# Optimization experiments

Hardware: AMD Instinct MI355X
Metric: run time of the kernel (lower is better)

## Reference

```python
import jax, jax.numpy as jnp
import numpy as np
import math

IMG = 224
PATCH = 14
E = 1024          # transformer width (ViT-L/14)
H = 16            # num heads
DH = E // H       # head dim
LAYERS = 24
FF = 4 * E        # CLIP MLP hidden
NROI = 32         # number of ROI bboxes
NSIDE = IMG // PATCH
NPATCH = NSIDE * NSIDE  # 256
T = 1 + NPATCH    # sequence length incl. CLS
INIT = 0.02
EPS_LN = 1e-5


def setup_inputs() -> dict:
    key = jax.random.key(0)
    ks = jax.random.split(key, 16)
    frame = jax.random.uniform(ks[0], (3, IMG, IMG), dtype=jnp.float32)
    # valid bboxes in pixel coords: x1<x2, y1<y2
    c = jax.random.uniform(ks[1], (NROI, 2), dtype=jnp.float32) * (IMG - 40.0) + 20.0
    s = jax.random.uniform(ks[2], (NROI, 2), dtype=jnp.float32) * 60.0 + 20.0
    bboxes = jnp.stack([c[:, 0] - s[:, 0] / 2, c[:, 1] - s[:, 1] / 2,
                        c[:, 0] + s[:, 0] / 2, c[:, 1] + s[:, 1] / 2], axis=-1)
    bboxes = jnp.clip(bboxes, 0.0, float(IMG))
    f32 = jnp.float32
    conv_w = jax.random.normal(ks[3], (E, 3, PATCH, PATCH), f32) * INIT
    cls_emb = jax.random.normal(ks[4], (E,), f32) * INIT
    wq = jax.random.normal(ks[5], (LAYERS, E, E), f32) * INIT
    wk = jax.random.normal(ks[6], (LAYERS, E, E), f32) * INIT
    wv = jax.random.normal(ks[7], (LAYERS, E, E), f32) * INIT
    wo = jax.random.normal(ks[8], (LAYERS, E, E), f32) * INIT
    bq = jnp.zeros((LAYERS, E), f32); bk = jnp.zeros((LAYERS, E), f32)
    bv = jnp.zeros((LAYERS, E), f32); bo = jnp.zeros((LAYERS, E), f32)
    ln1_s = jnp.ones((LAYERS, E), f32); ln1_b = jnp.zeros((LAYERS, E), f32)
    ln2_s = jnp.ones((LAYERS, E), f32); ln2_b = jnp.zeros((LAYERS, E), f32)
    w1 = jax.random.normal(ks[9], (LAYERS, E, FF), f32) * INIT
    b1 = jnp.zeros((LAYERS, FF), f32)
    w2 = jax.random.normal(ks[10], (LAYERS, FF, E), f32) * INIT
    b2 = jnp.zeros((LAYERS, E), f32)
    return {"frame": frame, "bboxes": bboxes, "conv_w": conv_w, "cls_emb": cls_emb,
            "ln1_s": ln1_s, "ln1_b": ln1_b, "wq": wq, "bq": bq, "wk": wk, "bk": bk,
            "wv": wv, "bv": bv, "wo": wo, "bo": bo, "ln2_s": ln2_s, "ln2_b": ln2_b,
            "w1": w1, "b1": b1, "w2": w2, "b2": b2}


def _patch_coords():
    r = jnp.arange(NSIDE, dtype=jnp.float32)
    c = jnp.arange(NSIDE, dtype=jnp.float32)
    cc, rr = jnp.meshgrid(c, r)  # row-major like the python loop
    x1 = (cc * PATCH).reshape(-1); y1 = (rr * PATCH).reshape(-1)
    return jnp.stack([x1, y1, x1 + PATCH, y1 + PATCH], axis=-1)  # (NPATCH,4)


def _overlap_ratio(bboxes, patches):
    # intersection area / patch area -> Mi (N, NPATCH)
    bx1, by1, bx2, by2 = [bboxes[:, None, i] for i in range(4)]
    px1, py1, px2, py2 = [patches[None, :, i] for i in range(4)]
    iw = jnp.clip(jnp.minimum(bx2, px2) - jnp.maximum(bx1, px1), 0.0)
    ih = jnp.clip(jnp.minimum(by2, py2) - jnp.maximum(by1, py1), 0.0)
    parea = (px2 - px1) * (py2 - py1)
    return iw * ih / parea


def _ln(x, s, b):
    m = jnp.mean(x, axis=-1, keepdims=True)
    v = jnp.var(x, axis=-1, keepdims=True)
    return (x - m) * jax.lax.rsqrt(v + EPS_LN) * s + b


def _quick_gelu(x):
    return x * jax.nn.sigmoid(1.702 * x)


def _forward(frame, bboxes, conv_w, cls_emb, ln1_s, ln1_b, wq, bq, wk, bk,
             wv, bv, wo, bo, ln2_s, ln2_b, w1, b1, w2, b2):
    # patch embed: conv stride=PATCH, then relu (as in module forward)
    x = jax.lax.conv_general_dilated(frame[None], conv_w, (PATCH, PATCH), 'VALID',
                                     dimension_numbers=('NCHW', 'OIHW', 'NCHW'))
    x = jax.nn.relu(x)                      # (1, E, NSIDE, NSIDE)
    x = x.reshape(E, NPATCH).T              # (NPATCH, E)
    x = jnp.concatenate([cls_emb[None, :], x], axis=0)  # (T, E)

    Mi = _overlap_ratio(bboxes, _patch_coords())  # (NROI, NPATCH)
    pb = Mi.sum(axis=0)
    pb = pb / (pb.max() + 1e-6)
    attn_bias = jnp.zeros((T, T), jnp.float32).at[0, 1:].set(pb)

    scale = 1.0 / math.sqrt(DH)

    def blk(x, p):
        l1s, l1b, Wq, Bq, Wk, Bk, Wv, Bv, Wo, Bo, l2s, l2b, W1, B1, W2, B2 = p
        h = _ln(x, l1s, l1b)
        q = (h @ Wq + Bq).reshape(T, H, DH)
        k = (h @ Wk + Bk).reshape(T, H, DH)
        v = (h @ Wv + Bv).reshape(T, H, DH)
        scores = jnp.einsum('lhd,shd->hls', q, k) * scale + attn_bias[None]
        a = jax.nn.softmax(scores, axis=-1)
        o = jnp.einsum('hls,shd->lhd', a, v).reshape(T, E) @ Wo + Bo
        x = x + o
        h2 = _ln(x, l2s, l2b)
        m = _quick_gelu(h2 @ W1 + B1) @ W2 + B2
        return x + m, None

    x, _ = jax.lax.scan(blk, x, (ln1_s, ln1_b, wq, bq, wk, bk, wv, bv, wo, bo,
                                 ln2_s, ln2_b, w1, b1, w2, b2))

    cls_out = x[0:1]            # (1, E)
    patch_out = x[1:]           # (NPATCH, E)
    roi = Mi @ patch_out        # (NROI, E)
    return jnp.concatenate([cls_out, roi], axis=0)  # (1+NROI, E)


def reference(frame, bboxes, conv_w, cls_emb, ln1_s, ln1_b, wq, bq, wk, bk,
              wv, bv, wo, bo, ln2_s, ln2_b, w1, b1, w2, b2):
    return _forward(frame, bboxes, conv_w, cls_emb, ln1_s, ln1_b, wq, bq, wk, bk,
                    wv, bv, wo, bo, ln2_s, ln2_b, w1, b1, w2, b2)
```

## Files before the change

kernel.cpp:

```cpp
#include <hip/hip_runtime.h>
#include <hip/hip_bf16.h>
#include <math.h>

#define E_DIM 1024
#define FF_DIM 4096
#define LAYERS 24
#define MPAD 384
#define SPAD 288
#define KCP 608

typedef __attribute__((ext_vector_type(8))) short short8;
typedef __attribute__((ext_vector_type(8))) __bf16 bf16x8;
typedef __attribute__((ext_vector_type(4))) float float4_t;
typedef __attribute__((ext_vector_type(4))) unsigned short ushort4_t;

union ABu { short8 s; bf16x8 b; };
union BFU { __bf16 b; unsigned short u; };

__device__ __forceinline__ float4_t MFMAs(short8 a, short8 b, float4_t c) {
  ABu ua, ub; ua.s = a; ub.s = b;
  return __builtin_amdgcn_mfma_f32_16x16x32_bf16(ua.b, ub.b, c, 0, 0, 0);
}
__device__ __forceinline__ unsigned short f2bf(float f) {
  BFU x; x.b = (__bf16)f; return x.u;
}

__global__ void prep_kernel(const float* __restrict__ frame, const float* __restrict__ conv_w,
                            unsigned short* __restrict__ Pm, unsigned short* __restrict__ Wp,
                            unsigned short* __restrict__ h, unsigned short* __restrict__ ob,
                            unsigned short* __restrict__ vTb) {
  int b = blockIdx.x, tid = threadIdx.x;
  if (b < 256) {
    int pr = b >> 4, pc = b & 15;
    for (int kk = tid; kk < KCP; kk += 256) {
      unsigned short us = 0;
      if (kk < 588) {
        int c = kk / 196, rem = kk % 196;
        int i = rem / 14, j = rem % 14;
        us = f2bf(frame[c * 224 * 224 + (pr * 14 + i) * 224 + (pc * 14 + j)]);
      }
      Pm[b * KCP + kk] = us;
    }
  } else if (b < 1280) {
    int n = b - 256;
    for (int kk = tid; kk < KCP; kk += 256) {
      unsigned short us = (kk < 588) ? f2bf(conv_w[n * 588 + kk]) : (unsigned short)0;
      Wp[n * KCP + kk] = us;
    }
  } else {
    int idx = (b - 1280) * 256 + tid;
    const int NH = (MPAD - 257) * E_DIM;
    const int NO = (MPAD - 272) * E_DIM;
    const int NV = 16 * 64 * (SPAD - 272);
    if (idx < NH) {
      h[257 * E_DIM + idx] = 0;
    } else if (idx < NH + NO) {
      ob[272 * E_DIM + (idx - NH)] = 0;
    } else if (idx < NH + NO + NV) {
      int i = idx - NH - NO;
      vTb[(size_t)(i >> 4) * SPAD + 272 + (i & 15)] = 0;
    }
  }
}

__global__ void pb_cls_kernel(const float* __restrict__ bboxes, const float* __restrict__ cls_emb,
                              float* __restrict__ pb, float* __restrict__ Mi, float* __restrict__ x) {
  __shared__ float sb[128];
  __shared__ float red[256];
  int tid = threadIdx.x;
  if (tid < 128) sb[tid] = bboxes[tid];
  __syncthreads();
  int p = tid;
  float px1 = (float)((p & 15) * 14), py1 = (float)((p >> 4) * 14);
  float px2 = px1 + 14.f, py2 = py1 + 14.f;
  float s = 0.f;
  for (int r = 0; r < 32; ++r) {
    float bx1 = sb[r * 4 + 0], by1 = sb[r * 4 + 1], bx2 = sb[r * 4 + 2], by2 = sb[r * 4 + 3];
    float iw = fmaxf(fminf(bx2, px2) - fmaxf(bx1, px1), 0.f);
    float ih = fmaxf(fminf(by2, py2) - fmaxf(by1, py1), 0.f);
    float ov = iw * ih * (1.f / 196.f);
    Mi[r * 256 + p] = ov;
    s += ov;
  }
  red[tid] = s;
  __syncthreads();
  for (int off = 128; off > 0; off >>= 1) {
    if (tid < off) red[tid] = fmaxf(red[tid], red[tid + off]);
    __syncthreads();
  }
  pb[p] = s / (red[0] + 1e-6f);
  for (int j = 0; j < 4; ++j) x[tid * 4 + j] = cls_emb[tid * 4 + j];
}

__global__ __launch_bounds__(256) void conv_gemm(const unsigned short* __restrict__ Pm,
                                                 const unsigned short* __restrict__ Wp,
                                                 float* __restrict__ x) {
  int n0 = blockIdx.x * 16;
  int tid = threadIdx.x, wave = tid >> 6, lane = tid & 63;
  int lg = lane >> 4, lc = lane & 15;
  float4_t acc[4] = {{0,0,0,0},{0,0,0,0},{0,0,0,0},{0,0,0,0}};
  const unsigned short* bp = Wp + (size_t)(n0 + lc) * KCP + lg * 8;
  const unsigned short* apt[4];
#pragma unroll
  for (int t = 0; t < 4; ++t) apt[t] = Pm + (size_t)((wave + t * 4) * 16 + lc) * KCP + lg * 8;
  for (int s = 0; s < 19; ++s) {
    short8 bf = *(const short8*)bp; bp += 32;
#pragma unroll
    for (int t = 0; t < 4; ++t) {
      short8 af = *(const short8*)apt[t]; apt[t] += 32;
      acc[t] = MFMAs(af, bf, acc[t]);
    }
  }
#pragma unroll
  for (int t = 0; t < 4; ++t) {
    int mbase = (wave + t * 4) * 16 + lg * 4;
#pragma unroll
    for (int r = 0; r < 4; ++r)
      x[(size_t)(1 + mbase + r) * E_DIM + n0 + lc] = fmaxf(acc[t][r], 0.f);
  }
}

#define WAITB(n) asm volatile("s_waitcnt vmcnt(" #n ") lgkmcnt(0)\n\ts_barrier" ::: "memory")
#define WAITV(n) asm volatile("s_waitcnt vmcnt(" #n ")" ::: "memory")

template <int NTOT, int EPI, int NK>
__global__ __launch_bounds__(256, 1) void gemm_nk(
    const unsigned short* __restrict__ A, int lda,
    const float* __restrict__ Wa, const float* __restrict__ Wb2, const float* __restrict__ Wc,
    const float* __restrict__ ba, const float* __restrict__ bb, const float* __restrict__ bc,
    int NNT,
    unsigned short* __restrict__ oq, unsigned short* __restrict__ okk,
    unsigned short* __restrict__ ovT, unsigned short* __restrict__ om,
    float* __restrict__ opart) {
  static_assert(NK == 2 || NK >= 3, "NK>=2");
  __shared__ __align__(16) char WbT[3 * 8192];
  int b = blockIdx.x;
  int p = ((b >> 4) << 3) | (b & 7);
  int mh = (b >> 3) & 1;
  int nt = p % NNT, ks = p / NNT;

  int tid = threadIdx.x, wave = tid >> 6, lane = tid & 63;
  int lg = lane >> 4, lc = lane & 15;

  const float* W; const float* bias; int ncl;
  if (EPI == 0) {
    int sel = nt >> 5; ncl = (nt & 31) << 5;
    W = (sel == 0) ? Wa : ((sel == 1) ? Wb2 : Wc);
    bias = (sel == 0) ? ba : ((sel == 1) ? bb : bc);
  } else {
    ncl = nt << 5; W = Wa; bias = ba;
  }

  const int kb0 = ks * (NK * 128);

  const int scol = tid & 31, rg = tid >> 5;
  const int skey = (scol & 7) * 16;
  const float* gsrc = W + (size_t)(kb0 + rg * 16) * NTOT + ncl + scol;
  const int wo0 = scol * 256 + ((rg * 32) ^ skey);
  const int wo1 = scol * 256 + ((rg * 32 + 16) ^ skey);

  const unsigned short* ap[3];
#pragma unroll
  for (int j = 0; j < 3; ++j) {
    int t0 = mh * 12 + wave * 3 + j;
    ap[j] = A + (size_t)(t0 * 16 + lc) * lda + kb0 + lg * 8;
  }

  float4_t acc[6];
#pragma unroll
  for (int i = 0; i < 6; ++i) acc[i] = (float4_t){0, 0, 0, 0};

  float g[2][16];
  short8 av[2][12];
  const int keyr = (lc & 7) * 16;

#define ISSUE_G(slot, t) { _Pragma("unroll") for (int j = 0; j < 16; ++j) \
    g[slot][j] = gsrc[(size_t)(t) * 128 * NTOT + (size_t)j * NTOT]; }
#define ISSUE_A(slot, t) { _Pragma("unroll") for (int s = 0; s < 4; ++s) \
    _Pragma("unroll") for (int j = 0; j < 3; ++j) \
      av[slot][s * 3 + j] = *(const short8*)(ap[j] + (size_t)(t) * 128 + s * 32); }
#define WRITE_G(slot, t) { short8 wlo, whi; \
    _Pragma("unroll") for (int j = 0; j < 8; ++j) { \
      wlo[j] = (short)f2bf(g[slot][j]); whi[j] = (short)f2bf(g[slot][8 + j]); } \
    char* dstb = WbT + ((t) % 3) * 8192; \
    *(short8*)(dstb + wo0) = wlo; \
    *(short8*)(dstb + wo1) = whi; }
#define COMP(t) { const char* ldsb = WbT + ((t) % 3) * 8192; \
    _Pragma("unroll") for (int s = 0; s < 4; ++s) { \
      int o = (s * 64 + lg * 16) ^ keyr; \
      short8 wf0 = *(const short8*)(ldsb + lc * 256 + o); \
      short8 wf1 = *(const short8*)(ldsb + (lc + 16) * 256 + o); \
      _Pragma("unroll") for (int j = 0; j < 3; ++j) { \
        acc[j * 2 + 0] = MFMAs(wf0, av[(t) & 1][s * 3 + j], acc[j * 2 + 0]); \
        acc[j * 2 + 1] = MFMAs(wf1, av[(t) & 1][s * 3 + j], acc[j * 2 + 1]); } } }

  if constexpr (NK == 2) {
    ISSUE_G(0, 0) ISSUE_G(1, 1) ISSUE_A(0, 0) ISSUE_A(1, 1)
    WAITV(24);
    WRITE_G(0, 0) WRITE_G(1, 1)
    asm volatile("s_waitcnt lgkmcnt(0)\n\ts_barrier" ::: "memory");
    WAITV(12);
    COMP(0)
    WAITV(0);
    COMP(1)
  } else {
    ISSUE_G(0, 0) ISSUE_G(1, 1) ISSUE_A(0, 0)
    WAITV(28);
    WRITE_G(0, 0)
    ISSUE_G(0, 2) ISSUE_A(1, 1)
#pragma unroll
    for (int t = 0; t < NK; ++t) {
      if (t <= NK - 3)      { WAITB(28); }
      else if (t == NK - 2) { WAITB(12); }
      else                  { WAITB(0);  }
      if (t + 1 < NK) WRITE_G((t + 1) & 1, t + 1)
      COMP(t)
      if (t + 3 < NK) ISSUE_G((t + 3) & 1, t + 3)
      if (t + 2 < NK) ISSUE_A(t & 1, t + 2)
    }
  }
#undef ISSUE_G
#undef ISSUE_A
#undef WRITE_G
#undef COMP

  float4_t bv0 = {0,0,0,0}, bv1 = {0,0,0,0};
  if (bias) {
    bv0 = *(const float4_t*)(bias + ncl + lg * 4);
    bv1 = *(const float4_t*)(bias + ncl + 16 + lg * 4);
  }

  if (EPI == 0) {
    int sel = nt >> 5;
    int head = ncl >> 6;
    int db0 = (ncl & 63) + lg * 4;
    int db1 = (ncl & 63) + 16 + lg * 4;
#pragma unroll
    for (int j = 0; j < 3; ++j) {
      int tile = mh * 12 + wave * 3 + j;
      int m = tile * 16 + lc;
      if (sel < 2) {
        unsigned short* dst = (sel == 0 ? oq : okk) + ((size_t)(head * MPAD + m)) * 64;
        ushort4_t h0, h1;
#pragma unroll
        for (int r = 0; r < 4; ++r) {
          h0[r] = f2bf(acc[j * 2 + 0][r] + bv0[r]);
          h1[r] = f2bf(acc[j * 2 + 1][r] + bv1[r]);
        }
        *(ushort4_t*)(dst + db0) = h0;
        *(ushort4_t*)(dst + db1) = h1;
      } else if (tile < 17) {
#pragma unroll
        for (int r = 0; r < 4; ++r) {
          ovT[(size_t)(head * 64 + db0 + r) * SPAD + m] = f2bf(acc[j * 2 + 0][r] + bv0[r]);
          ovT[(size_t)(head * 64 + db1 + r) * SPAD + m] = f2bf(acc[j * 2 + 1][r] + bv1[r]);
        }
      }
    }
  } else if (EPI == 1) {
#pragma unroll
    for (int j = 0; j < 3; ++j) {
      int m = (mh * 12 + wave * 3 + j) * 16 + lc;
      ushort4_t h0, h1;
#pragma unroll
      for (int r = 0; r < 4; ++r) {
        float v0 = acc[j * 2 + 0][r] + bv0[r];
        float v1 = acc[j * 2 + 1][r] + bv1[r];
        h0[r] = f2bf(v0 / (1.f + __expf(-1.702f * v0)));
        h1[r] = f2bf(v1 / (1.f + __expf(-1.702f * v1)));
      }
      *(ushort4_t*)(om + (size_t)m * FF_DIM + ncl + lg * 4) = h0;
      *(ushort4_t*)(om + (size_t)m * FF_DIM + ncl + 16 + lg * 4) = h1;
    }
  } else {
#pragma unroll
    for (int j = 0; j < 3; ++j) {
      int m = (mh * 12 + wave * 3 + j) * 16 + lc;
      float* dst = opart + ((size_t)ks * MPAD + m) * E_DIM + ncl + lg * 4;
      *(float4_t*)dst = acc[j * 2 + 0];
      *(float4_t*)(dst + 16) = acc[j * 2 + 1];
    }
  }
}

__global__ __launch_bounds__(256) void attn_kernel(
    const unsigned short* __restrict__ qb, const unsigned short* __restrict__ kb,
    const unsigned short* __restrict__ vT, const float* __restrict__ pb,
    unsigned short* __restrict__ ob) {
  int head = blockIdx.x / 17, qt = blockIdx.x % 17;
  int q0 = qt * 16;
  int tid = threadIdx.x, wave = tid >> 6, lane = tid & 63;
  int lg = lane >> 4, lc = lane & 15;
  const unsigned short* qh = qb + (size_t)head * MPAD * 64;
  const unsigned short* kh = kb + (size_t)head * MPAD * 64;
  const unsigned short* vh = vT + (size_t)head * 64 * SPAD;

  short8 aq0 = *(const short8*)(qh + (size_t)(q0 + lc) * 64 + lg * 8);
  short8 aq1 = *(const short8*)(qh + (size_t)(q0 + lc) * 64 + 32 + lg * 8);

  float4_t sc[5];
  int st[5]; int nst = 0;
#pragma unroll
  for (int j = 0; j < 5; ++j) {
    int t = wave + j * 4;
    st[j] = (t < 17) ? t : 0;
    if (t < 17) nst = j + 1;
    sc[j] = (float4_t){0,0,0,0};
  }
#pragma unroll
  for (int j = 0; j < 5; ++j) {
    if (j < nst) {
      const unsigned short* kp = kh + (size_t)(st[j] * 16 + lc) * 64 + lg * 8;
      short8 b0 = *(const short8*)kp;
      short8 b1 = *(const short8*)(kp + 32);
      sc[j] = MFMAs(aq0, b0, sc[j]);
      sc[j] = MFMAs(aq1, b1, sc[j]);
    }
  }
  float mx[4] = {-1e30f, -1e30f, -1e30f, -1e30f};
#pragma unroll
  for (int j = 0; j < 5; ++j) {
    if (j < nst) {
      int sg = st[j] * 16 + lc;
#pragma unroll
      for (int r = 0; r < 4; ++r) {
        float v = sc[j][r] * 0.125f;
        if (sg >= 257) v = -1e30f;
        else if (q0 + lg * 4 + r == 0 && sg >= 1) v += pb[sg - 1];
        sc[j][r] = v;
        mx[r] = fmaxf(mx[r], v);
      }
    }
  }
#pragma unroll
  for (int r = 0; r < 4; ++r) {
    mx[r] = fmaxf(mx[r], __shfl_xor(mx[r], 1, 64));
    mx[r] = fmaxf(mx[r], __shfl_xor(mx[r], 2, 64));
    mx[r] = fmaxf(mx[r], __shfl_xor(mx[r], 4, 64));
    mx[r] = fmaxf(mx[r], __shfl_xor(mx[r], 8, 64));
  }
  __shared__ float smax[4][16];
  __shared__ float sden[4][16];
  __shared__ __align__(16) unsigned short P[16][SPAD];
  if (lc == 0) {
#pragma unroll
    for (int r = 0; r < 4; ++r) smax[wave][lg * 4 + r] = mx[r];
  }
  __syncthreads();
  float fm[4], den[4] = {0, 0, 0, 0};
#pragma unroll
  for (int r = 0; r < 4; ++r) {
    int qq = lg * 4 + r;
    fm[r] = fmaxf(fmaxf(smax[0][qq], smax[1][qq]), fmaxf(smax[2][qq], smax[3][qq]));
  }
#pragma unroll
  for (int j = 0; j < 5; ++j) {
    if (j < nst) {
#pragma unroll
      for (int r = 0; r < 4; ++r) {
        float pe = __expf(sc[j][r] - fm[r]);
        sc[j][r] = pe;
        den[r] += pe;
      }
    }
  }
#pragma unroll
  for (int r = 0; r < 4; ++r) {
    den[r] += __shfl_xor(den[r], 1, 64);
    den[r] += __shfl_xor(den[r], 2, 64);
    den[r] += __shfl_xor(den[r], 4, 64);
    den[r] += __shfl_xor(den[r], 8, 64);
  }
  if (lc == 0) {
#pragma unroll
    for (int r = 0; r < 4; ++r) sden[wave][lg * 4 + r] = den[r];
  }
  P[tid >> 4][272 + (tid & 15)] = 0;
#pragma unroll
  for (int j = 0; j < 5; ++j) {
    if (j < nst) {
#pragma unroll
      for (int r = 0; r < 4; ++r) P[lg * 4 + r][st[j] * 16 + lc] = f2bf(sc[j][r]);
    }
  }
  __syncthreads();
  float denf[4];
#pragma unroll
  for (int r = 0; r < 4; ++r) {
    int qq = lg * 4 + r;
    denf[r] = sden[0][qq] + sden[1][qq] + sden[2][qq] + sden[3][qq];
  }
  int d0 = wave * 16;
  float4_t oa = {0, 0, 0, 0};
#pragma unroll
  for (int s9 = 0; s9 < 9; ++s9) {
    short8 pa = *(const short8*)(&P[lc][s9 * 32 + lg * 8]);
    short8 bv = *(const short8*)(vh + (size_t)(d0 + lc) * SPAD + s9 * 32 + lg * 8);
    oa = MFMAs(pa, bv, oa);
  }
#pragma unroll
  for (int r = 0; r < 4; ++r) {
    int qg = q0 + lg * 4 + r;
    ob[(size_t)qg * E_DIM + head * 64 + d0 + lc] = f2bf(oa[r] / denf[r]);
  }
}

__global__ __launch_bounds__(256) void reduce_ln_kernel(
    float* __restrict__ x, const float* __restrict__ part, int nparts,
    const float* __restrict__ rbias,
    const float* __restrict__ lns, const float* __restrict__ lnb,
    unsigned short* __restrict__ hout) {
  int m = blockIdx.x, tid = threadIdx.x;
  int c0 = tid * 4;
  float4_t v = *(const float4_t*)(x + (size_t)m * E_DIM + c0);
  if (rbias) v += *(const float4_t*)(rbias + c0);
  for (int s = 0; s < nparts; ++s)
    v += *(const float4_t*)(part + ((size_t)s * MPAD + m) * E_DIM + c0);
  if (nparts > 0) *(float4_t*)(x + (size_t)m * E_DIM + c0) = v;
  float s1 = v[0] + v[1] + v[2] + v[3];
  float s2 = v[0] * v[0] + v[1] * v[1] + v[2] * v[2] + v[3] * v[3];
#pragma unroll
  for (int off = 1; off < 64; off <<= 1) {
    s1 += __shfl_xor(s1, off, 64);
    s2 += __shfl_xor(s2, off, 64);
  }
  __shared__ float red[8];
  int wave = tid >> 6, lane = tid & 63;
  if (lane == 0) { red[wave * 2] = s1; red[wave * 2 + 1] = s2; }
  __syncthreads();
  s1 = red[0] + red[2] + red[4] + red[6];
  s2 = red[1] + red[3] + red[5] + red[7];
  float mean = s1 * (1.f / 1024.f);
  float var = s2 * (1.f / 1024.f) - mean * mean;
  float rstd = rsqrtf(var + 1e-5f);
  float4_t ls = *(const float4_t*)(lns + c0);
  float4_t lb = *(const float4_t*)(lnb + c0);
  ushort4_t hv;
#pragma unroll
  for (int r = 0; r < 4; ++r) hv[r] = f2bf((v[r] - mean) * rstd * ls[r] + lb[r]);
  *(ushort4_t*)(hout + (size_t)m * E_DIM + c0) = hv;
}

__global__ __launch_bounds__(256) void roi_kernel(const float* __restrict__ x,
                                                  const float* __restrict__ Mi,
                                                  float* __restrict__ out) {
  int b = blockIdx.x, tid = threadIdx.x;
  int c0 = tid * 4;
  if (b == 0) {
    *(float4_t*)(out + c0) = *(const float4_t*)(x + c0);
  } else {
    __shared__ float mi[256];
    mi[tid] = Mi[(b - 1) * 256 + tid];
    __syncthreads();
    float4_t acc = {0, 0, 0, 0};
    for (int p = 0; p < 256; ++p) {
      float4_t xv = *(const float4_t*)(x + (size_t)(1 + p) * E_DIM + c0);
      acc += mi[p] * xv;
    }
    *(float4_t*)(out + (size_t)b * E_DIM + c0) = acc;
  }
}

extern "C" void kernel_launch(void* const* d_in, const int* in_sizes, int n_in,
                              void* d_out, int out_size, void* d_ws, size_t ws_size,
                              hipStream_t stream) {
  const float* frame   = (const float*)d_in[0];
  const float* bboxes  = (const float*)d_in[1];
  const float* conv_w  = (const float*)d_in[2];
  const float* cls_emb = (const float*)d_in[3];
  const float* ln1_s   = (const float*)d_in[4];
  const float* ln1_b   = (const float*)d_in[5];
  const float* wq = (const float*)d_in[6];
  const float* bq = (const float*)d_in[7];
  const float* wk = (const float*)d_in[8];
  const float* bk = (const float*)d_in[9];
  const float* wv = (const float*)d_in[10];
  const float* bv = (const float*)d_in[11];
  const float* wo = (const float*)d_in[12];
  const float* bo = (const float*)d_in[13];
  const float* ln2_s = (const float*)d_in[14];
  const float* ln2_b = (const float*)d_in[15];
  const float* w1 = (const float*)d_in[16];
  const float* b1 = (const float*)d_in[17];
  const float* w2 = (const float*)d_in[18];
  const float* b2 = (const float*)d_in[19];

  char* base = (char*)d_ws;
  auto carve = [&](size_t bytes) {
    char* r = base;
    base += (bytes + 255) & ~(size_t)255;
    return r;
  };
  float* x            = (float*)carve((size_t)257 * E_DIM * 4);
  unsigned short* h   = (unsigned short*)carve((size_t)MPAD * E_DIM * 2);
  unsigned short* qb  = (unsigned short*)carve((size_t)16 * MPAD * 64 * 2);
  unsigned short* kbf = (unsigned short*)carve((size_t)16 * MPAD * 64 * 2);
  unsigned short* vTb = (unsigned short*)carve((size_t)16 * 64 * SPAD * 2);
  unsigned short* ob  = (unsigned short*)carve((size_t)MPAD * E_DIM * 2);
  unsigned short* mb  = (unsigned short*)carve((size_t)MPAD * FF_DIM * 2);
  float* part         = (float*)carve((size_t)4 * MPAD * E_DIM * 4);
  float* pbv          = (float*)carve(256 * 4);
  float* Mi           = (float*)carve(32 * 256 * 4);
  unsigned short* Pm  = (unsigned short*)carve((size_t)256 * KCP * 2);
  unsigned short* Wp  = (unsigned short*)carve((size_t)1024 * KCP * 2);

  prep_kernel<<<1280 + 1020, 256, 0, stream>>>(frame, conv_w, Pm, Wp, h, ob, vTb);
  pb_cls_kernel<<<1, 256, 0, stream>>>(bboxes, cls_emb, pbv, Mi, x);
  conv_gemm<<<64, 256, 0, stream>>>(Pm, Wp, x);
  reduce_ln_kernel<<<257, 256, 0, stream>>>(x, nullptr, 0, nullptr, ln1_s, ln1_b, h);

  for (int l = 0; l < LAYERS; ++l) {
    size_t o2  = (size_t)l * E_DIM * E_DIM;
    size_t o1  = (size_t)l * E_DIM;
    size_t of1 = (size_t)l * E_DIM * FF_DIM;
    size_t ofb = (size_t)l * FF_DIM;
    gemm_nk<1024, 0, 8><<<192, 256, 0, stream>>>(h, E_DIM, wq + o2, wk + o2, wv + o2,
                                                 bq + o1, bk + o1, bv + o1,
                                                 96, qb, kbf, vTb, nullptr, nullptr);
    attn_kernel<<<272, 256, 0, stream>>>(qb, kbf, vTb, pbv, ob);
    gemm_nk<1024, 2, 2><<<256, 256, 0, stream>>>(ob, E_DIM, wo + o2, nullptr, nullptr,
                                                 nullptr, nullptr, nullptr,
                                                 32, nullptr, nullptr, nullptr, nullptr, part);
    reduce_ln_kernel<<<257, 256, 0, stream>>>(x, part, 4, bo + o1, ln2_s + o1, ln2_b + o1, h);
    gemm_nk<4096, 1, 8><<<256, 256, 0, stream>>>(h, E_DIM, w1 + of1, nullptr, nullptr,
                                                 b1 + ofb, nullptr, nullptr,
                                                 128, nullptr, nullptr, nullptr, mb, nullptr);
    gemm_nk<1024, 2, 8><<<256, 256, 0, stream>>>(mb, FF_DIM, w2 + of1, nullptr, nullptr,
                                                 nullptr, nullptr, nullptr,
                                                 32, nullptr, nullptr, nullptr, nullptr, part);
    const float* nls = (l < LAYERS - 1) ? (ln1_s + (size_t)(l + 1) * E_DIM) : ln1_s;
    const float* nlb = (l < LAYERS - 1) ? (ln1_b + (size_t)(l + 1) * E_DIM) : ln1_b;
    reduce_ln_kernel<<<257, 256, 0, stream>>>(x, part, 4, b2 + o1, nls, nlb, h);
  }
  roi_kernel<<<33, 256, 0, stream>>>(x, Mi, (float*)d_out);
}
```

Baseline: 1.800 ms.

## Store split-K partials in bf16, spread conv GEMM, reorder compute before LDS write

Split-K partial sums from the Wo and W2 GEMMs are now written as bf16 instead of fp32, and reduce_ln reads them back as bf16. This halves the partial-buffer traffic on every layer, at the cost of lower precision in the residual accumulation. The conv GEMM now launches four times as many blocks, each handling one M tile per wave, to raise parallelism. In the pipelined GEMM loop, the MFMA compute is moved ahead of the LDS write for the next stage.

```diff
diff --git a/kernel.cpp b/kernel.cpp
--- a/kernel.cpp
+++ b/kernel.cpp
@@ -23,6 +23,9 @@
 }
 __device__ __forceinline__ unsigned short f2bf(float f) {
   BFU x; x.b = (__bf16)f; return x.u;
+}
+__device__ __forceinline__ float bf2f(unsigned short u) {
+  BFU x; x.u = u; return (float)x.b;
 }
 
 __global__ void prep_kernel(const float* __restrict__ frame, const float* __restrict__ conv_w,
@@ -95,29 +98,23 @@
 __global__ __launch_bounds__(256) void conv_gemm(const unsigned short* __restrict__ Pm,
                                                  const unsigned short* __restrict__ Wp,
                                                  float* __restrict__ x) {
-  int n0 = blockIdx.x * 16;
+  int nb = blockIdx.x & 63, mq = blockIdx.x >> 6;
+  int n0 = nb * 16;
   int tid = threadIdx.x, wave = tid >> 6, lane = tid & 63;
   int lg = lane >> 4, lc = lane & 15;
-  float4_t acc[4] = {{0,0,0,0},{0,0,0,0},{0,0,0,0},{0,0,0,0}};
+  int mt = mq * 4 + wave;
+  float4_t acc = {0, 0, 0, 0};
   const unsigned short* bp = Wp + (size_t)(n0 + lc) * KCP + lg * 8;
-  const unsigned short* apt[4];
-#pragma unroll
-  for (int t = 0; t < 4; ++t) apt[t] = Pm + (size_t)((wave + t * 4) * 16 + lc) * KCP + lg * 8;
+  const unsigned short* ap = Pm + (size_t)(mt * 16 + lc) * KCP + lg * 8;
   for (int s = 0; s < 19; ++s) {
     short8 bf = *(const short8*)bp; bp += 32;
-#pragma unroll
-    for (int t = 0; t < 4; ++t) {
-      short8 af = *(const short8*)apt[t]; apt[t] += 32;
-      acc[t] = MFMAs(af, bf, acc[t]);
-    }
-  }
-#pragma unroll
-  for (int t = 0; t < 4; ++t) {
-    int mbase = (wave + t * 4) * 16 + lg * 4;
-#pragma unroll
-    for (int r = 0; r < 4; ++r)
-      x[(size_t)(1 + mbase + r) * E_DIM + n0 + lc] = fmaxf(acc[t][r], 0.f);
-  }
+    short8 af = *(const short8*)ap; ap += 32;
+    acc = MFMAs(af, bf, acc);
+  }
+  int mbase = mt * 16 + lg * 4;
+#pragma unroll
+  for (int r = 0; r < 4; ++r)
+    x[(size_t)(1 + mbase + r) * E_DIM + n0 + lc] = fmaxf(acc[r], 0.f);
 }
 
 #define WAITB(n) asm volatile("s_waitcnt vmcnt(" #n ") lgkmcnt(0)\n\ts_barrier" ::: "memory")
@@ -131,7 +128,7 @@
     int NNT,
     unsigned short* __restrict__ oq, unsigned short* __restrict__ okk,
     unsigned short* __restrict__ ovT, unsigned short* __restrict__ om,
-    float* __restrict__ opart) {
+    unsigned short* __restrict__ opart) {
   static_assert(NK == 2 || NK >= 3, "NK>=2");
   __shared__ __align__(16) char WbT[3 * 8192];
   int b = blockIdx.x;
@@ -213,8 +210,8 @@
       if (t <= NK - 3)      { WAITB(28); }
       else if (t == NK - 2) { WAITB(12); }
       else                  { WAITB(0);  }
+      COMP(t)
       if (t + 1 < NK) WRITE_G((t + 1) & 1, t + 1)
-      COMP(t)
       if (t + 3 < NK) ISSUE_G((t + 3) & 1, t + 3)
       if (t + 2 < NK) ISSUE_A(t & 1, t + 2)
     }
@@ -276,9 +273,15 @@
 #pragma unroll
     for (int j = 0; j < 3; ++j) {
       int m = (mh * 12 + wave * 3 + j) * 16 + lc;
-      float* dst = opart + ((size_t)ks * MPAD + m) * E_DIM + ncl + lg * 4;
-      *(float4_t*)dst = acc[j * 2 + 0];
-      *(float4_t*)(dst + 16) = acc[j * 2 + 1];
+      unsigned short* dst = opart + ((size_t)ks * MPAD + m) * E_DIM + ncl + lg * 4;
+      ushort4_t h0, h1;
+#pragma unroll
+      for (int r = 0; r < 4; ++r) {
+        h0[r] = f2bf(acc[j * 2 + 0][r]);
+        h1[r] = f2bf(acc[j * 2 + 1][r]);
+      }
+      *(ushort4_t*)dst = h0;
+      *(ushort4_t*)(dst + 16) = h1;
     }
   }
 }
@@ -406,7 +409,7 @@
 }
 
 __global__ __launch_bounds__(256) void reduce_ln_kernel(
-    float* __restrict__ x, const float* __restrict__ part, int nparts,
+    float* __restrict__ x, const unsigned short* __restrict__ part, int nparts,
     const float* __restrict__ rbias,
     const float* __restrict__ lns, const float* __restrict__ lnb,
     unsigned short* __restrict__ hout) {
@@ -414,8 +417,11 @@
   int c0 = tid * 4;
   float4_t v = *(const float4_t*)(x + (size_t)m * E_DIM + c0);
   if (rbias) v += *(const float4_t*)(rbias + c0);
-  for (int s = 0; s < nparts; ++s)
-    v += *(const float4_t*)(part + ((size_t)s * MPAD + m) * E_DIM + c0);
+  for (int s = 0; s < nparts; ++s) {
+    ushort4_t pv = *(const ushort4_t*)(part + ((size_t)s * MPAD + m) * E_DIM + c0);
+#pragma unroll
+    for (int r = 0; r < 4; ++r) v[r] += bf2f(pv[r]);
+  }
   if (nparts > 0) *(float4_t*)(x + (size_t)m * E_DIM + c0) = v;
   float s1 = v[0] + v[1] + v[2] + v[3];
   float s2 = v[0] * v[0] + v[1] * v[1] + v[2] * v[2] + v[3] * v[3];
@@ -498,7 +504,7 @@
   unsigned short* vTb = (unsigned short*)carve((size_t)16 * 64 * SPAD * 2);
   unsigned short* ob  = (unsigned short*)carve((size_t)MPAD * E_DIM * 2);
   unsigned short* mb  = (unsigned short*)carve((size_t)MPAD * FF_DIM * 2);
-  float* part         = (float*)carve((size_t)4 * MPAD * E_DIM * 4);
+  unsigned short* part= (unsigned short*)carve((size_t)4 * MPAD * E_DIM * 2);
   float* pbv          = (float*)carve(256 * 4);
   float* Mi           = (float*)carve(32 * 256 * 4);
   unsigned short* Pm  = (unsigned short*)carve((size_t)256 * KCP * 2);
@@ -506,7 +512,7 @@
 
   prep_kernel<<<1280 + 1020, 256, 0, stream>>>(frame, conv_w, Pm, Wp, h, ob, vTb);
   pb_cls_kernel<<<1, 256, 0, stream>>>(bboxes, cls_emb, pbv, Mi, x);
-  conv_gemm<<<64, 256, 0, stream>>>(Pm, Wp, x);
+  conv_gemm<<<256, 256, 0, stream>>>(Pm, Wp, x);
   reduce_ln_kernel<<<257, 256, 0, stream>>>(x, nullptr, 0, nullptr, ln1_s, ln1_b, h);
 
   for (int l = 0; l < LAYERS; ++l) {
```

After: 1.799 ms. About the same (-0.0%).
